# Performance work log

Hardware: AMD Instinct MI355X
Metric: run time of the kernel (lower is better)

## Reference

```python
import jax, jax.numpy as jnp
import numpy as np

HEADS = 16
D_MODEL = 1024
D_FF = 4096
D_K = D_MODEL // HEADS
EPS = 1e-5


def layer_norm(x, g, b):
    mu = jnp.mean(x, axis=-1, keepdims=True)
    var = jnp.mean(jnp.square(x - mu), axis=-1, keepdims=True)
    return (x - mu) * jax.lax.rsqrt(var + EPS) * g + b


def setup_inputs() -> dict:
    key = jax.random.key(0)
    ks = jax.random.split(key, 12)
    B, S = 2, 2048
    s = 0.02
    return {
        "x": jax.random.normal(ks[0], (B, S, D_MODEL), jnp.float32),
        "mask": jnp.zeros((B, 1, 1, S), jnp.bool_),
        "W_Q": jax.random.normal(ks[1], (D_MODEL, D_MODEL), jnp.float32) * s,
        "W_K": jax.random.normal(ks[2], (D_MODEL, D_MODEL), jnp.float32) * s,
        "W_V": jax.random.normal(ks[3], (D_MODEL, D_MODEL), jnp.float32) * s,
        "W_O": jax.random.normal(ks[4], (D_MODEL, D_MODEL), jnp.float32) * s,
        "W1": jax.random.normal(ks[5], (D_FF, D_MODEL), jnp.float32) * s,
        "b1": jnp.zeros((D_FF,), jnp.float32),
        "W2": jax.random.normal(ks[6], (D_MODEL, D_FF), jnp.float32) * s,
        "b2": jnp.zeros((D_MODEL,), jnp.float32),
        "g1": jnp.ones((D_MODEL,), jnp.float32),
        "beta1": jnp.zeros((D_MODEL,), jnp.float32),
        "g2": jnp.ones((D_MODEL,), jnp.float32),
        "beta2": jnp.zeros((D_MODEL,), jnp.float32),
    }


def reference(x, mask, W_Q, W_K, W_V, W_O, W1, b1, W2, b2, g1, beta1, g2, beta2):
    B, S, _ = x.shape
    # pre-LN block (pre_ln=True)
    res = x
    h = layer_norm(x, g1, beta1)
    # torch Linear: y = h @ W.T
    q = (h @ W_Q.T).reshape(B, S, HEADS, D_K).transpose(0, 2, 1, 3)  # [B,H,S,dk]
    k = (h @ W_K.T).reshape(B, S, HEADS, D_K).transpose(0, 2, 1, 3)
    v = (h @ W_V.T).reshape(B, S, HEADS, D_K).transpose(0, 2, 1, 3)
    e = jnp.einsum("bhqd,bhkd->bhqk", q, k) / jnp.sqrt(jnp.float32(D_K))
    e = jnp.where(mask, -jnp.inf, e)
    w = jax.nn.softmax(e, axis=-1)
    a = jnp.einsum("bhqk,bhkd->bhqd", w, v)
    a = a.transpose(0, 2, 1, 3).reshape(B, S, D_MODEL)
    o = a @ W_O.T
    x = o + res  # dropout identity in eval
    # FFN sub-block
    res = x
    h = layer_norm(x, g2, beta2)
    # faithful to source: Linear -> Linear -> ReLU (ReLU at the end)
    f = jax.nn.relu((h @ W1.T + b1) @ W2.T + b2)
    return f + res
```

## Files before the change

kernel.cpp:

```cpp
#include <hip/hip_runtime.h>

typedef __attribute__((ext_vector_type(8))) short short8;
typedef __attribute__((ext_vector_type(4))) float f32x4;

typedef const void __attribute__((address_space(1)))* gas_ptr;
typedef void __attribute__((address_space(3)))* las_ptr;

__device__ __forceinline__ void gl16(const void* g, void* l) {
    __builtin_amdgcn_global_load_lds((gas_ptr)g, (las_ptr)l, 16, 0, 0);
}

__device__ __forceinline__ void tile_barrier() {
    __builtin_amdgcn_sched_barrier(0);
    asm volatile("s_waitcnt vmcnt(0)" ::: "memory");
    __builtin_amdgcn_s_barrier();
    __builtin_amdgcn_sched_barrier(0);
}

__device__ __forceinline__ unsigned short f2bf(float f) {
    union { float f; unsigned u; } v; v.f = f;
    unsigned r = v.u + 0x7FFFu + ((v.u >> 16) & 1u);
    return (unsigned short)(r >> 16);
}
__device__ __forceinline__ float exp2_fast(float x) {
    float r; asm("v_exp_f32 %0, %1" : "=v"(r) : "v"(x)); return r;
}
__device__ __forceinline__ unsigned cvtpk(float lo, float hi) {
    unsigned r; asm("v_cvt_pk_bf16_f32 %0, %1, %2" : "=v"(r) : "v"(lo), "v"(hi)); return r;
}

#define QSCALE 0.18033688011112042f

__global__ __launch_bounds__(256) void cvt6_kernel(const float* __restrict__ W_Q,
                                                   const float* __restrict__ W_K,
                                                   const float* __restrict__ W_V,
                                                   const float* __restrict__ W_O,
                                                   const float* __restrict__ W1,
                                                   const float* __restrict__ W2,
                                                   unsigned short* __restrict__ out) {
    int i = blockIdx.x * blockDim.x + threadIdx.x;
    const int stride = gridDim.x * blockDim.x;
    for (; i < 3145728; i += stride) {
        const float* src;
        int off;
        if (i < 1048576) {
            src = (i < 262144) ? W_Q : (i < 524288) ? W_K : (i < 786432) ? W_V : W_O;
            off = i & 262143;
        } else {
            const int j = i - 1048576;
            src = (j < 1048576) ? W1 : W2;
            off = j & 1048575;
        }
        const float4 v = ((const float4*)src)[off];
        ushort4 o;
        o.x = f2bf(v.x); o.y = f2bf(v.y); o.z = f2bf(v.z); o.w = f2bf(v.w);
        ((ushort4*)out)[i] = o;
    }
}

__global__ __launch_bounds__(256) void ln_kernel(const float* __restrict__ x,
                                                 const float* __restrict__ g,
                                                 const float* __restrict__ bta,
                                                 unsigned short* __restrict__ out) {
    const int row = blockIdx.x, t = threadIdx.x;
    const float4 v = ((const float4*)(x + (size_t)row * 1024))[t];
    float s  = v.x + v.y + v.z + v.w;
    float s2 = v.x * v.x + v.y * v.y + v.z * v.z + v.w * v.w;
    for (int m = 1; m <= 32; m <<= 1) {
        s  += __shfl_xor(s, m);
        s2 += __shfl_xor(s2, m);
    }
    __shared__ float red[8];
    const int wid = t >> 6, lane = t & 63;
    if (lane == 0) { red[wid] = s; red[4 + wid] = s2; }
    __syncthreads();
    s  = red[0] + red[1] + red[2] + red[3];
    s2 = red[4] + red[5] + red[6] + red[7];
    const float mu  = s * (1.0f / 1024.0f);
    const float var = s2 * (1.0f / 1024.0f) - mu * mu;
    const float r   = rsqrtf(var + 1e-5f);
    const float4 gv = ((const float4*)g)[t];
    const float4 bv = ((const float4*)bta)[t];
    ushort4 o;
    o.x = f2bf((v.x - mu) * r * gv.x + bv.x);
    o.y = f2bf((v.y - mu) * r * gv.y + bv.y);
    o.z = f2bf((v.z - mu) * r * gv.z + bv.z);
    o.w = f2bf((v.w - mu) * r * gv.w + bv.w);
    ((ushort4*)(out + (size_t)row * 1024))[t] = o;
}

template <int EPI, int BN>
__global__ __launch_bounds__(256) void gemm_bt(const unsigned short* __restrict__ A,
                                               const unsigned short* __restrict__ B,
                                               const float* __restrict__ bias,
                                               const float* __restrict__ res,
                                               void* __restrict__ out,
                                               int M, int N, int K) {
    __shared__ unsigned short As[2][128 * 64];
    __shared__ unsigned short Bs[2][BN * 64];
    const int t = threadIdx.x;
    const int m0 = blockIdx.x * 128, n0 = blockIdx.y * BN;
    const int lane = t & 63, wid = t >> 6;
    const int wr = wid >> 1, wc = wid & 1;
    const int fr = lane & 15, fq = lane >> 4;
    const int NJ = BN / 32;
    const int NBJ = BN / 32;

    f32x4 acc[4][NJ] = {};

    const int srow = t >> 3;
    const int lelem = ((t & 7) ^ (srow & 7)) << 3;
    size_t aoff[4], boff[NBJ];
#pragma unroll
    for (int j = 0; j < 4; ++j)
        aoff[j] = (size_t)(m0 + srow + j * 32) * K + lelem;
#pragma unroll
    for (int j = 0; j < NBJ; ++j)
        boff[j] = (size_t)(n0 + srow + j * 32) * K + lelem;

    auto stage = [&](int k0, int buf) {
#pragma unroll
        for (int j = 0; j < 4; ++j)
            gl16(&A[aoff[j] + k0], &As[buf][(t + j * 256) * 8]);
#pragma unroll
        for (int j = 0; j < NBJ; ++j)
            gl16(&B[boff[j] + k0], &Bs[buf][(t + j * 256) * 8]);
    };

    const int swz = (fr & 7) << 4;
    const int arow = (wr * 64 + fr) * 128;
    const int brow = (wc * (BN / 2) + fr) * 128;

    stage(0, 0);
    int buf = 0;
    for (int k0 = 0; k0 < K; k0 += 64) {
        tile_barrier();
        if (k0 + 64 < K) stage(k0 + 64, buf ^ 1);
        const char* abase = (const char*)&As[buf][0] + arow;
        const char* bbase = (const char*)&Bs[buf][0] + brow;
#pragma unroll
        for (int kk = 0; kk < 2; ++kk) {
            const int ib = ((kk << 6) | (fq << 4)) ^ swz;
            short8 af[4], bf[NJ];
#pragma unroll
            for (int i = 0; i < 4; ++i)
                af[i] = *(const short8*)(abase + i * 16 * 128 + ib);
#pragma unroll
            for (int j = 0; j < NJ; ++j)
                bf[j] = *(const short8*)(bbase + j * 16 * 128 + ib);
#pragma unroll
            for (int i = 0; i < 4; ++i)
#pragma unroll
                for (int j = 0; j < NJ; ++j)
                    acc[i][j] = __builtin_amdgcn_mfma_f32_16x16x32_bf16(af[i], bf[j], acc[i][j], 0, 0, 0);
        }
        buf ^= 1;
    }

#pragma unroll
    for (int i = 0; i < 4; ++i)
#pragma unroll
        for (int j = 0; j < NJ; ++j)
#pragma unroll
            for (int q = 0; q < 4; ++q) {
                const int row = m0 + wr * 64 + i * 16 + fq * 4 + q;
                const int col = n0 + wc * (BN / 2) + j * 16 + fr;
                const size_t idx = (size_t)row * N + col;
                float v = acc[i][j][q];
                if (EPI == 0) {
                    ((unsigned short*)out)[idx] = f2bf(v);
                } else if (EPI == 1) {
                    ((unsigned short*)out)[idx] = f2bf(v + bias[col]);
                } else if (EPI == 2) {
                    ((float*)out)[idx] = v + res[idx];
                } else if (EPI == 3) {
                    float u = v + bias[col];
                    u = u > 0.0f ? u : 0.0f;
                    ((float*)out)[idx] = u + res[idx];
                } else {
                    ((unsigned short*)out)[idx] = f2bf(col < 1024 ? v * QSCALE : v);
                }
            }
}

__global__ __launch_bounds__(256, 2) void attn_kernel(const unsigned short* __restrict__ qk,
                                                      const unsigned short* __restrict__ vt,
                                                      unsigned short* __restrict__ out) {
    __shared__ unsigned short Kls[2][4096];

    const int t = threadIdx.x, lane = t & 63, w = t >> 6;
    const int fr = lane & 15, fq = lane >> 4;
    const int flat = blockIdx.x;
    const int xcd = flat & 7, slot = flat >> 3;
    const int bh = xcd * 4 + (slot >> 4);
    const int qx = slot & 15;
    const int b = bh >> 4, h = bh & 15;
    const size_t tokbase = (size_t)b * 2048;
    const int q0 = qx * 128 + w * 32;

    short8 qf[2][2];
#pragma unroll
    for (int qt = 0; qt < 2; ++qt)
#pragma unroll
        for (int c = 0; c < 2; ++c)
            qf[qt][c] = *(const short8*)&qk[(tokbase + q0 + qt * 16 + fr) * 2048 + h * 64 + c * 32 + fq * 8];

    const int krow = t >> 3;
    const int kcolb = ((t & 7) << 4) ^ ((krow & 7) << 4);
    const unsigned short* ksrc = qk + (tokbase + krow) * 2048 + 1024 + h * 64 + (kcolb >> 1);
    const unsigned short* vsrc = vt + (size_t)(h * 64 + fr) * 4096 + tokbase + fq * 8;

    const int sw = (fr & 7) << 4;
    const int kb0 = fr * 128 + ((fq * 16) ^ sw);

    f32x4 acc[2][4] = {};
    float lrun[2] = {0.0f, 0.0f};

    auto stageK = [&](int kv, int buf) {
        gl16(ksrc + (size_t)kv * 2048, &Kls[buf][t * 8]);
        gl16(ksrc + (size_t)(kv + 32) * 2048, &Kls[buf][2048 + t * 8]);
    };

    stageK(0, 0);
    asm volatile("s_waitcnt vmcnt(0)" ::: "memory");
    __builtin_amdgcn_s_barrier();

    int cur = 0;
    for (int kv0 = 0; kv0 < 2048; kv0 += 64) {
        short8 vf[2][4];
#pragma unroll
        for (int c2 = 0; c2 < 2; ++c2)
#pragma unroll
            for (int dt = 0; dt < 4; ++dt)
                vf[c2][dt] = *(const short8*)&vsrc[(size_t)dt * 16 * 4096 + kv0 + c2 * 32];
        if (kv0 + 64 < 2048) stageK(kv0 + 64, cur ^ 1);
        __builtin_amdgcn_sched_barrier(0);

        const char* kbase = (const char*)&Kls[cur][0];
        short8 ka[4][2];
#pragma unroll
        for (int kh = 0; kh < 4; ++kh)
#pragma unroll
            for (int c = 0; c < 2; ++c)
                ka[kh][c] = *(const short8*)(kbase + kh * 2048 + (kb0 ^ (c * 64)));

#pragma unroll
        for (int qt = 0; qt < 2; ++qt) {
            f32x4 e0 = {}, e1 = {}, e2 = {}, e3 = {};
            e0 = __builtin_amdgcn_mfma_f32_16x16x32_bf16(ka[0][0], qf[qt][0], e0, 0, 0, 0);
            e0 = __builtin_amdgcn_mfma_f32_16x16x32_bf16(ka[0][1], qf[qt][1], e0, 0, 0, 0);
            e1 = __builtin_amdgcn_mfma_f32_16x16x32_bf16(ka[1][0], qf[qt][0], e1, 0, 0, 0);
            e1 = __builtin_amdgcn_mfma_f32_16x16x32_bf16(ka[1][1], qf[qt][1], e1, 0, 0, 0);
            e2 = __builtin_amdgcn_mfma_f32_16x16x32_bf16(ka[2][0], qf[qt][0], e2, 0, 0, 0);
            e2 = __builtin_amdgcn_mfma_f32_16x16x32_bf16(ka[2][1], qf[qt][1], e2, 0, 0, 0);
            e3 = __builtin_amdgcn_mfma_f32_16x16x32_bf16(ka[3][0], qf[qt][0], e3, 0, 0, 0);
            e3 = __builtin_amdgcn_mfma_f32_16x16x32_bf16(ka[3][1], qf[qt][1], e3, 0, 0, 0);

            float p[16];
#pragma unroll
            for (int i = 0; i < 4; ++i) {
                p[i]      = exp2_fast(e0[i]);
                p[4 + i]  = exp2_fast(e1[i]);
                p[8 + i]  = exp2_fast(e2[i]);
                p[12 + i] = exp2_fast(e3[i]);
            }
            lrun[qt] += (((p[0] + p[1]) + (p[2] + p[3])) + ((p[4] + p[5]) + (p[6] + p[7])))
                      + (((p[8] + p[9]) + (p[10] + p[11])) + ((p[12] + p[13]) + (p[14] + p[15])));

#pragma unroll
            for (int c2 = 0; c2 < 2; ++c2) {
                const float* pp = p + c2 * 8;
                const unsigned w0 = cvtpk(pp[0], pp[1]);
                const unsigned w1 = cvtpk(pp[2], pp[3]);
                const unsigned w2 = cvtpk(pp[4], pp[5]);
                const unsigned w3 = cvtpk(pp[6], pp[7]);
                const int s0 = ((fq & 1) << 5) + fr;
                const int s1 = s0 + 16;
                const unsigned a0 = __shfl(w0, s0), a1 = __shfl(w1, s0);
                const unsigned a2 = __shfl(w0, s1), a3 = __shfl(w1, s1);
                const unsigned b0 = __shfl(w2, s0), b1 = __shfl(w3, s0);
                const unsigned b2 = __shfl(w2, s1), b3 = __shfl(w3, s1);
                union { unsigned u[4]; short8 s; } pu;
                const bool lohalf = (fq < 2);
                pu.u[0] = lohalf ? a0 : b0;
                pu.u[1] = lohalf ? a1 : b1;
                pu.u[2] = lohalf ? a2 : b2;
                pu.u[3] = lohalf ? a3 : b3;
                const short8 pf = pu.s;
#pragma unroll
                for (int dt = 0; dt < 4; ++dt)
                    acc[qt][dt] = __builtin_amdgcn_mfma_f32_16x16x32_bf16(pf, vf[c2][dt], acc[qt][dt], 0, 0, 0);
            }
        }

        asm volatile("s_waitcnt vmcnt(0)" ::: "memory");
        __builtin_amdgcn_s_barrier();
        cur ^= 1;
    }

#pragma unroll
    for (int qt = 0; qt < 2; ++qt) {
        float lr = lrun[qt];
        lr += __shfl_xor(lr, 16);
        lr += __shfl_xor(lr, 32);
        const float linv = 1.0f / lr;
        float li[4];
#pragma unroll
        for (int i = 0; i < 4; ++i) li[i] = __shfl(linv, fq * 4 + i);
#pragma unroll
        for (int dt = 0; dt < 4; ++dt)
#pragma unroll
            for (int i = 0; i < 4; ++i)
                out[(tokbase + q0 + qt * 16 + fq * 4 + i) * 1024 + h * 64 + dt * 16 + fr] =
                    f2bf(acc[qt][dt][i] * li[i]);
    }
}

extern "C" void kernel_launch(void* const* d_in, const int* in_sizes, int n_in,
                              void* d_out, int out_size, void* d_ws, size_t ws_size,
                              hipStream_t stream) {
    const float* x     = (const float*)d_in[0];
    const float* W_Q   = (const float*)d_in[2];
    const float* W_K   = (const float*)d_in[3];
    const float* W_V   = (const float*)d_in[4];
    const float* W_O   = (const float*)d_in[5];
    const float* W1    = (const float*)d_in[6];
    const float* b1    = (const float*)d_in[7];
    const float* W2    = (const float*)d_in[8];
    const float* b2    = (const float*)d_in[9];
    const float* g1    = (const float*)d_in[10];
    const float* beta1 = (const float*)d_in[11];
    const float* g2    = (const float*)d_in[12];
    const float* beta2 = (const float*)d_in[13];

    const int TOK = 4096, DM = 1024, DFF = 4096;

    unsigned short* wsu = (unsigned short*)d_ws;
    unsigned short* wq  = wsu;
    unsigned short* wk  = wq + 1048576;
    unsigned short* wv  = wk + 1048576;
    unsigned short* wo  = wv + 1048576;
    unsigned short* w1  = wo + 1048576;
    unsigned short* w2  = w1 + 4194304;
    unsigned short* hln = w2 + 4194304;
    unsigned short* qkb = hln + 4194304;
    unsigned short* vt  = qkb + 8388608;
    unsigned short* ab  = vt + 4194304;
    float* x1           = (float*)(ab + 4194304);
    unsigned short* t1  = (unsigned short*)(x1 + 4194304);

    cvt6_kernel<<<2048, 256, 0, stream>>>(W_Q, W_K, W_V, W_O, W1, W2, wq);

    ln_kernel<<<TOK, 256, 0, stream>>>(x, g1, beta1, hln);

    gemm_bt<4, 128><<<dim3(TOK / 128, 2048 / 128), 256, 0, stream>>>(hln, wq, nullptr, nullptr, qkb, TOK, 2048, DM);
    gemm_bt<0, 64><<<dim3(DM / 128, TOK / 64), 256, 0, stream>>>(wv, hln, nullptr, nullptr, vt, DM, TOK, DM);

    attn_kernel<<<512, 256, 0, stream>>>(qkb, vt, ab);

    gemm_bt<2, 64><<<dim3(TOK / 128, DM / 64), 256, 0, stream>>>(ab, wo, nullptr, x, x1, TOK, DM, DM);

    ln_kernel<<<TOK, 256, 0, stream>>>(x1, g2, beta2, hln);

    gemm_bt<1, 128><<<dim3(TOK / 128, DFF / 128), 256, 0, stream>>>(hln, w1, b1, nullptr, t1, TOK, DFF, DM);
    gemm_bt<3, 64><<<dim3(TOK / 128, DM / 64), 256, 0, stream>>>(t1, w2, b2, x1, d_out, TOK, DM, DFF);
}
```

Measured before the change: 246.8 us.

## Switch attention kernel to 32x32x16 MFMA with permlane32 swap for P layout

```diff
diff --git a/kernel.cpp b/kernel.cpp
--- a/kernel.cpp
+++ b/kernel.cpp
@@ -2,19 +2,13 @@
 
 typedef __attribute__((ext_vector_type(8))) short short8;
 typedef __attribute__((ext_vector_type(4))) float f32x4;
+typedef __attribute__((ext_vector_type(16))) float f32x16;
 
 typedef const void __attribute__((address_space(1)))* gas_ptr;
 typedef void __attribute__((address_space(3)))* las_ptr;
 
 __device__ __forceinline__ void gl16(const void* g, void* l) {
     __builtin_amdgcn_global_load_lds((gas_ptr)g, (las_ptr)l, 16, 0, 0);
-}
-
-__device__ __forceinline__ void tile_barrier() {
-    __builtin_amdgcn_sched_barrier(0);
-    asm volatile("s_waitcnt vmcnt(0)" ::: "memory");
-    __builtin_amdgcn_s_barrier();
-    __builtin_amdgcn_sched_barrier(0);
 }
 
 __device__ __forceinline__ unsigned short f2bf(float f) {
@@ -27,6 +21,9 @@
 }
 __device__ __forceinline__ unsigned cvtpk(float lo, float hi) {
     unsigned r; asm("v_cvt_pk_bf16_f32 %0, %1, %2" : "=v"(r) : "v"(lo), "v"(hi)); return r;
+}
+__device__ __forceinline__ void pswap(unsigned& a, unsigned& b) {
+    asm("v_permlane32_swap_b32 %0, %1" : "+v"(a), "+v"(b));
 }
 
 #define QSCALE 0.18033688011112042f
@@ -134,7 +131,10 @@
     stage(0, 0);
     int buf = 0;
     for (int k0 = 0; k0 < K; k0 += 64) {
-        tile_barrier();
+        __builtin_amdgcn_sched_barrier(0);
+        asm volatile("s_waitcnt vmcnt(0)" ::: "memory");
+        __builtin_amdgcn_s_barrier();
+        __builtin_amdgcn_sched_barrier(0);
         if (k0 + 64 < K) stage(k0 + 64, buf ^ 1);
         const char* abase = (const char*)&As[buf][0] + arow;
         const char* bbase = (const char*)&Bs[buf][0] + brow;
@@ -189,7 +189,7 @@
     __shared__ unsigned short Kls[2][4096];
 
     const int t = threadIdx.x, lane = t & 63, w = t >> 6;
-    const int fr = lane & 15, fq = lane >> 4;
+    const int il = lane & 31, ih = lane >> 5;
     const int flat = blockIdx.x;
     const int xcd = flat & 7, slot = flat >> 3;
     const int bh = xcd * 4 + (slot >> 4);
@@ -198,23 +198,20 @@
     const size_t tokbase = (size_t)b * 2048;
     const int q0 = qx * 128 + w * 32;
 
-    short8 qf[2][2];
-#pragma unroll
-    for (int qt = 0; qt < 2; ++qt)
-#pragma unroll
-        for (int c = 0; c < 2; ++c)
-            qf[qt][c] = *(const short8*)&qk[(tokbase + q0 + qt * 16 + fr) * 2048 + h * 64 + c * 32 + fq * 8];
+    short8 qf[4];
+#pragma unroll
+    for (int s = 0; s < 4; ++s)
+        qf[s] = *(const short8*)&qk[(tokbase + q0 + il) * 2048 + h * 64 + s * 16 + ih * 8];
 
     const int krow = t >> 3;
     const int kcolb = ((t & 7) << 4) ^ ((krow & 7) << 4);
     const unsigned short* ksrc = qk + (tokbase + krow) * 2048 + 1024 + h * 64 + (kcolb >> 1);
-    const unsigned short* vsrc = vt + (size_t)(h * 64 + fr) * 4096 + tokbase + fq * 8;
-
-    const int sw = (fr & 7) << 4;
-    const int kb0 = fr * 128 + ((fq * 16) ^ sw);
-
-    f32x4 acc[2][4] = {};
-    float lrun[2] = {0.0f, 0.0f};
+    const unsigned short* vsrc = vt + (size_t)(h * 64 + il) * 4096 + tokbase + ih * 8;
+
+    const int kswz = (il & 7) << 4;
+
+    f32x16 oacc[2] = {};
+    float lrun = 0.0f;
 
     auto stageK = [&](int kv, int buf) {
         gl16(ksrc + (size_t)kv * 2048, &Kls[buf][t * 8]);
@@ -227,69 +224,49 @@
 
     int cur = 0;
     for (int kv0 = 0; kv0 < 2048; kv0 += 64) {
-        short8 vf[2][4];
-#pragma unroll
-        for (int c2 = 0; c2 < 2; ++c2)
-#pragma unroll
-            for (int dt = 0; dt < 4; ++dt)
-                vf[c2][dt] = *(const short8*)&vsrc[(size_t)dt * 16 * 4096 + kv0 + c2 * 32];
+        short8 vb[2][4];
+#pragma unroll
+        for (int dt = 0; dt < 2; ++dt)
+#pragma unroll
+            for (int kc = 0; kc < 4; ++kc)
+                vb[dt][kc] = *(const short8*)&vsrc[(size_t)(dt * 32) * 4096 + kv0 + kc * 16];
         if (kv0 + 64 < 2048) stageK(kv0 + 64, cur ^ 1);
         __builtin_amdgcn_sched_barrier(0);
 
         const char* kbase = (const char*)&Kls[cur][0];
-        short8 ka[4][2];
-#pragma unroll
-        for (int kh = 0; kh < 4; ++kh)
-#pragma unroll
-            for (int c = 0; c < 2; ++c)
-                ka[kh][c] = *(const short8*)(kbase + kh * 2048 + (kb0 ^ (c * 64)));
-
-#pragma unroll
-        for (int qt = 0; qt < 2; ++qt) {
-            f32x4 e0 = {}, e1 = {}, e2 = {}, e3 = {};
-            e0 = __builtin_amdgcn_mfma_f32_16x16x32_bf16(ka[0][0], qf[qt][0], e0, 0, 0, 0);
-            e0 = __builtin_amdgcn_mfma_f32_16x16x32_bf16(ka[0][1], qf[qt][1], e0, 0, 0, 0);
-            e1 = __builtin_amdgcn_mfma_f32_16x16x32_bf16(ka[1][0], qf[qt][0], e1, 0, 0, 0);
-            e1 = __builtin_amdgcn_mfma_f32_16x16x32_bf16(ka[1][1], qf[qt][1], e1, 0, 0, 0);
-            e2 = __builtin_amdgcn_mfma_f32_16x16x32_bf16(ka[2][0], qf[qt][0], e2, 0, 0, 0);
-            e2 = __builtin_amdgcn_mfma_f32_16x16x32_bf16(ka[2][1], qf[qt][1], e2, 0, 0, 0);
-            e3 = __builtin_amdgcn_mfma_f32_16x16x32_bf16(ka[3][0], qf[qt][0], e3, 0, 0, 0);
-            e3 = __builtin_amdgcn_mfma_f32_16x16x32_bf16(ka[3][1], qf[qt][1], e3, 0, 0, 0);
+#pragma unroll
+        for (int c32 = 0; c32 < 2; ++c32) {
+            short8 ka[4];
+#pragma unroll
+            for (int s = 0; s < 4; ++s)
+                ka[s] = *(const short8*)(kbase + (c32 * 32 + il) * 128 +
+                                         (((s * 32) | (ih * 16)) ^ kswz));
+            f32x16 e = {};
+#pragma unroll
+            for (int s = 0; s < 4; ++s)
+                e = __builtin_amdgcn_mfma_f32_32x32x16_bf16(ka[s], qf[s], e, 0, 0, 0);
 
             float p[16];
 #pragma unroll
-            for (int i = 0; i < 4; ++i) {
-                p[i]      = exp2_fast(e0[i]);
-                p[4 + i]  = exp2_fast(e1[i]);
-                p[8 + i]  = exp2_fast(e2[i]);
-                p[12 + i] = exp2_fast(e3[i]);
-            }
-            lrun[qt] += (((p[0] + p[1]) + (p[2] + p[3])) + ((p[4] + p[5]) + (p[6] + p[7])))
-                      + (((p[8] + p[9]) + (p[10] + p[11])) + ((p[12] + p[13]) + (p[14] + p[15])));
-
-#pragma unroll
-            for (int c2 = 0; c2 < 2; ++c2) {
-                const float* pp = p + c2 * 8;
-                const unsigned w0 = cvtpk(pp[0], pp[1]);
-                const unsigned w1 = cvtpk(pp[2], pp[3]);
-                const unsigned w2 = cvtpk(pp[4], pp[5]);
-                const unsigned w3 = cvtpk(pp[6], pp[7]);
-                const int s0 = ((fq & 1) << 5) + fr;
-                const int s1 = s0 + 16;
-                const unsigned a0 = __shfl(w0, s0), a1 = __shfl(w1, s0);
-                const unsigned a2 = __shfl(w0, s1), a3 = __shfl(w1, s1);
-                const unsigned b0 = __shfl(w2, s0), b1 = __shfl(w3, s0);
-                const unsigned b2 = __shfl(w2, s1), b3 = __shfl(w3, s1);
-                union { unsigned u[4]; short8 s; } pu;
-                const bool lohalf = (fq < 2);
-                pu.u[0] = lohalf ? a0 : b0;
-                pu.u[1] = lohalf ? a1 : b1;
-                pu.u[2] = lohalf ? a2 : b2;
-                pu.u[3] = lohalf ? a3 : b3;
-                const short8 pf = pu.s;
-#pragma unroll
-                for (int dt = 0; dt < 4; ++dt)
-                    acc[qt][dt] = __builtin_amdgcn_mfma_f32_16x16x32_bf16(pf, vf[c2][dt], acc[qt][dt], 0, 0, 0);
+            for (int r = 0; r < 16; ++r) p[r] = exp2_fast(e[r]);
+            lrun += (((p[0] + p[1]) + (p[2] + p[3])) + ((p[4] + p[5]) + (p[6] + p[7])))
+                  + (((p[8] + p[9]) + (p[10] + p[11])) + ((p[12] + p[13]) + (p[14] + p[15])));
+
+            unsigned wd[8];
+#pragma unroll
+            for (int i = 0; i < 8; ++i) wd[i] = cvtpk(p[2 * i], p[2 * i + 1]);
+            pswap(wd[0], wd[2]);
+            pswap(wd[1], wd[3]);
+            pswap(wd[4], wd[6]);
+            pswap(wd[5], wd[7]);
+            union { unsigned u[4]; short8 s8; } pa0, pa1;
+            pa0.u[0] = wd[0]; pa0.u[1] = wd[1]; pa0.u[2] = wd[2]; pa0.u[3] = wd[3];
+            pa1.u[0] = wd[4]; pa1.u[1] = wd[5]; pa1.u[2] = wd[6]; pa1.u[3] = wd[7];
+
+#pragma unroll
+            for (int dt = 0; dt < 2; ++dt) {
+                oacc[dt] = __builtin_amdgcn_mfma_f32_32x32x16_bf16(pa0.s8, vb[dt][c32 * 2 + 0], oacc[dt], 0, 0, 0);
+                oacc[dt] = __builtin_amdgcn_mfma_f32_32x32x16_bf16(pa1.s8, vb[dt][c32 * 2 + 1], oacc[dt], 0, 0, 0);
             }
         }
 
@@ -298,22 +275,20 @@
         cur ^= 1;
     }
 
-#pragma unroll
-    for (int qt = 0; qt < 2; ++qt) {
-        float lr = lrun[qt];
-        lr += __shfl_xor(lr, 16);
-        lr += __shfl_xor(lr, 32);
-        const float linv = 1.0f / lr;
-        float li[4];
-#pragma unroll
-        for (int i = 0; i < 4; ++i) li[i] = __shfl(linv, fq * 4 + i);
-#pragma unroll
-        for (int dt = 0; dt < 4; ++dt)
-#pragma unroll
-            for (int i = 0; i < 4; ++i)
-                out[(tokbase + q0 + qt * 16 + fq * 4 + i) * 1024 + h * 64 + dt * 16 + fr] =
-                    f2bf(acc[qt][dt][i] * li[i]);
-    }
+    lrun += __shfl_xor(lrun, 32);
+    const float linv = 1.0f / lrun;
+    float li[16];
+#pragma unroll
+    for (int r = 0; r < 16; ++r)
+        li[r] = __shfl(linv, (r & 3) + 8 * (r >> 2) + 4 * ih);
+#pragma unroll
+    for (int dt = 0; dt < 2; ++dt)
+#pragma unroll
+        for (int r = 0; r < 16; ++r) {
+            const int qrow = (r & 3) + 8 * (r >> 2) + 4 * ih;
+            out[(tokbase + q0 + qrow) * 1024 + h * 64 + dt * 32 + il] =
+                f2bf(oacc[dt][r] * li[r]);
+        }
 }
 
 extern "C" void kernel_launch(void* const* d_in, const int* in_sizes, int n_in,
```

Result: no change. 244.7 us (-0.8%).
